# Performance work log

Hardware: AMD Instinct MI355X
Metric: run time of the kernel (lower is better)

Reference implementation:

```python
import jax, jax.numpy as jnp
import numpy as np

N = 100000   # nodes
E = 1600000  # edges
IN, HID, OUT = 128, 128, 64  # hidden = 2 * out_channels per GCNEncoder


def setup_inputs() -> dict:
    key = jax.random.key(0)
    k = jax.random.split(key, 5)
    x = jax.random.normal(k[0], (N, IN), dtype=jnp.float32)
    edge_index = jax.random.randint(k[1], (2, E), 0, N, dtype=jnp.int32)
    # Glorot-style init like PyG GCNConv
    W1 = jax.random.normal(k[2], (IN, HID), dtype=jnp.float32) * (1.0 / np.sqrt(IN))
    b1 = jnp.zeros((HID,), dtype=jnp.float32)
    W2 = jax.random.normal(k[3], (HID, OUT), dtype=jnp.float32) * (1.0 / np.sqrt(HID))
    b2 = jnp.zeros((OUT,), dtype=jnp.float32)
    return {"x": x, "edge_index": edge_index, "W1": W1, "b1": b1, "W2": W2, "b2": b2}


def gcn_conv(x, row, col, W, b):
    # x: [N, F_in]; row/col: [E+N] (edge_index with self-loops appended)
    h = x @ W                                      # dense transform [N, F_out]
    deg = jax.ops.segment_sum(jnp.ones_like(col, dtype=h.dtype), col, num_segments=N)
    dinv = jnp.where(deg > 0, jax.lax.rsqrt(deg), 0.0)
    norm = dinv[row] * dinv[col]                   # symmetric normalization per edge
    msg = h[row] * norm[:, None]                   # gather + scale: [E+N, F_out]
    out = jax.ops.segment_sum(msg, col, num_segments=N)  # scatter-add to targets
    return out + b


def reference(x, edge_index, W1, b1, W2, b2):
    loops = jnp.arange(N, dtype=edge_index.dtype)
    row = jnp.concatenate([edge_index[0], loops])  # sources
    col = jnp.concatenate([edge_index[1], loops])  # targets
    h = jax.nn.relu(gcn_conv(x, row, col, W1, b1))
    return gcn_conv(h, row, col, W2, b2)
```

## Files before the change

### kernel.cpp

```cpp
#include <hip/hip_runtime.h>
#include <hip/hip_fp16.h>

#define N_NODES 100000
#define N_EDGES 1600000
#define K_DIM   128

#define CHUNK_LG 7
#define CHUNK    128
#define NBKT     ((N_NODES + CHUNK - 1) / CHUNK)
#define CAP      2560
#define EPB      4096
#define NBLK_A   ((N_EDGES + EPB - 1) / EPB)
#define G1_BLOCKS ((N_NODES + 63) / 64)
#define NBLK_TOT (G1_BLOCKS + NBLK_A)

typedef _Float16 half8 __attribute__((ext_vector_type(8)));
typedef float    f32x4 __attribute__((ext_vector_type(4)));

__global__ __launch_bounds__(256) void k_prepW(const float* __restrict__ W1,
                                               const float* __restrict__ W2,
                                               _Float16* __restrict__ Wt1,
                                               _Float16* __restrict__ Wt2,
                                               int* __restrict__ gcur) {
    if (blockIdx.x >= 12) {
        int i = (blockIdx.x - 12) * 256 + threadIdx.x;
        if (i < NBKT) gcur[i] = 0;
        return;
    }
    int c = blockIdx.x * 256 + threadIdx.x;
    const float* W; _Float16* Wt; int nout;
    if (c < 2048) { W = W1; Wt = Wt1; nout = 128; }
    else          { W = W2; Wt = Wt2; nout = 64; c -= 2048; }
    int n  = c >> 4;
    int k0 = (c & 15) * 8;
    half8 v;
#pragma unroll
    for (int j = 0; j < 8; ++j)
        v[j] = (_Float16)W[(size_t)(k0 + j) * nout + n];
    *reinterpret_cast<half8*>(Wt + (size_t)n * K_DIM + k0) = v;
}

__global__ __launch_bounds__(256) void k_gemm1_bucket(
    const float* __restrict__ x, const _Float16* __restrict__ Wt,
    _Float16* __restrict__ Hout,
    const int* __restrict__ row, const int* __restrict__ col,
    int* __restrict__ gcur, int* __restrict__ pairs)
{
    __shared__ __align__(16) char smem[128 * 136 * 2];

    if (blockIdx.x % 5 != 0) {
        constexpr int KD = K_DIM, NOUT = 128, NT = NOUT / 16;
        _Float16 (*Blds)[KD + 8] = reinterpret_cast<_Float16(*)[KD + 8]>(smem);

        for (int i = threadIdx.x; i < NOUT * (KD / 8); i += 256) {
            int n = i >> 4, k0 = (i & 15) * 8;
            *reinterpret_cast<half8*>(&Blds[n][k0]) =
                *reinterpret_cast<const half8*>(Wt + (size_t)n * KD + k0);
        }
        __syncthreads();

        const int tile = blockIdx.x - blockIdx.x / 5 - 1;
        const int wave = threadIdx.x >> 6;
        const int lane = threadIdx.x & 63;
        const int r16  = lane & 15;
        const int kg   = lane >> 4;
        const int arow = tile * 64 + wave * 16 + r16;
        const bool rowok = arow < N_NODES;

        f32x4 acc[NT];
#pragma unroll
        for (int ct = 0; ct < NT; ++ct) acc[ct] = (f32x4){0.f, 0.f, 0.f, 0.f};

#pragma unroll
        for (int kc = 0; kc < KD / 32; ++kc) {
            const int k0 = kc * 32 + kg * 8;
            float4 xa = make_float4(0.f, 0.f, 0.f, 0.f), xb = xa;
            if (rowok) {
                const float4* ap = reinterpret_cast<const float4*>(
                    x + (size_t)arow * KD + k0);
                xa = ap[0]; xb = ap[1];
            }
            half8 a;
            a[0] = (_Float16)xa.x; a[1] = (_Float16)xa.y;
            a[2] = (_Float16)xa.z; a[3] = (_Float16)xa.w;
            a[4] = (_Float16)xb.x; a[5] = (_Float16)xb.y;
            a[6] = (_Float16)xb.z; a[7] = (_Float16)xb.w;
#pragma unroll
            for (int ct = 0; ct < NT; ++ct) {
                half8 b = *reinterpret_cast<const half8*>(&Blds[ct * 16 + r16][k0]);
                acc[ct] = __builtin_amdgcn_mfma_f32_16x16x32_f16(a, b, acc[ct], 0, 0, 0);
            }
        }

        const int orow0 = tile * 64 + wave * 16 + kg * 4;
#pragma unroll
        for (int r = 0; r < 4; ++r) {
            int orow = orow0 + r;
            if (orow < N_NODES) {
#pragma unroll
                for (int ct = 0; ct < NT; ++ct)
                    Hout[(size_t)orow * NOUT + ct * 16 + r16] = (_Float16)acc[ct][r];
            }
        }
    } else {
        int* hist  = (int*)smem;
        int* sbase = hist + 1024;
        int* lcur  = hist + 2048;
        int t = threadIdx.x;
        for (int i = t; i < NBKT; i += 256) { hist[i] = 0; lcur[i] = 0; }
        __syncthreads();
        int base = (blockIdx.x / 5) * EPB;
        int myb[16], myp[16];
#pragma unroll
        for (int j = 0; j < 16; ++j) {
            int i = base + t + j * 256;
            int b = -1, p = 0;
            if (i < N_EDGES) {
                int r = row[i], c = col[i];
                b = c >> CHUNK_LG;
                p = ((c & (CHUNK - 1)) << 17) | r;
                atomicAdd(&hist[b], 1);
            }
            myb[j] = b; myp[j] = p;
        }
        __syncthreads();
        for (int i = t; i < NBKT; i += 256) {
            int c = hist[i];
            sbase[i] = c ? atomicAdd(&gcur[i], c) : 0;
        }
        __syncthreads();
#pragma unroll
        for (int j = 0; j < 16; ++j) {
            int b = myb[j];
            if (b >= 0) {
                int pos = sbase[b] + atomicAdd(&lcur[b], 1);
                pairs[(size_t)b * CAP + pos] = myp[j];
            }
        }
    }
}

__global__ __launch_bounds__(256) void k_fillB(const int* __restrict__ gcur,
                                               const int* __restrict__ pairs,
                                               int* __restrict__ rowptr,
                                               float* __restrict__ dinv,
                                               int* __restrict__ srows) {
    __shared__ int mpl[CAP];
    __shared__ int red[256];
    __shared__ int psum[CHUNK];
    __shared__ int deg[CHUNK];
    __shared__ int curs[CHUNK];
    int b = blockIdx.x, t = threadIdx.x;

    int part = 0;
    for (int i = t; i < NBKT; i += 256)
        if (i < b) part += gcur[i];
    red[t] = part;
    if (t < CHUNK) deg[t] = 0;
    __syncthreads();
    for (int off = 128; off; off >>= 1) {
        if (t < off) red[t] += red[t + off];
        __syncthreads();
    }
    int gb = red[0];
    int cnt = gcur[b];
    if (b == 0 && t == 0) rowptr[N_NODES] = N_EDGES;

    const int* mp = pairs + (size_t)b * CAP;

    for (int i = t; i < cnt; i += 256) {
        int v = mp[i];
        mpl[i] = v;
        atomicAdd(&deg[v >> 17], 1);
    }
    __syncthreads();

    int d = (t < CHUNK) ? deg[t] : 0;
    if (t < CHUNK) psum[t] = d;
    __syncthreads();
    for (int off = 1; off < CHUNK; off <<= 1) {
        int u = (t >= off && t < CHUNK) ? psum[t - off] : 0;
        __syncthreads();
        if (t < CHUNK) psum[t] += u;
        __syncthreads();
    }
    if (t < CHUNK) {
        int o = gb + psum[t] - d;
        curs[t] = o;
        int node = (b << CHUNK_LG) + t;
        if (node < N_NODES) {
            rowptr[node] = o;
            dinv[node] = rsqrtf(1.f + (float)d);
        }
    }
    __syncthreads();
    for (int i = t; i < cnt; i += 256) {
        int v = mpl[i];
        int pos = atomicAdd(&curs[v >> 17], 1);
        srows[pos] = v & 0x1FFFF;
    }
}

template<int NOUT>
__global__ __launch_bounds__(256) void k_gemm_mfma2(
    const _Float16* __restrict__ Ah, const _Float16* __restrict__ Wt,
    const float* __restrict__ b_in, _Float16* __restrict__ Hout, int nrows)
{
    constexpr int KD = K_DIM;
    constexpr int NT = NOUT / 16;
    __shared__ _Float16 Blds[NOUT][KD + 8];

    for (int i = threadIdx.x; i < NOUT * (KD / 8); i += 256) {
        int n = i >> 4, k0 = (i & 15) * 8;
        *reinterpret_cast<half8*>(&Blds[n][k0]) =
            *reinterpret_cast<const half8*>(Wt + (size_t)n * KD + k0);
    }
    __syncthreads();

    const int wave = threadIdx.x >> 6;
    const int lane = threadIdx.x & 63;
    const int r16  = lane & 15;
    const int kg   = lane >> 4;
    const int arow = blockIdx.x * 64 + wave * 16 + r16;
    const bool rowok = arow < nrows;

    f32x4 acc[NT];
#pragma unroll
    for (int ct = 0; ct < NT; ++ct) acc[ct] = (f32x4){0.f, 0.f, 0.f, 0.f};

#pragma unroll
    for (int kc = 0; kc < KD / 32; ++kc) {
        const int k0 = kc * 32 + kg * 8;
        uint4 raw = make_uint4(0, 0, 0, 0);
        if (rowok)
            raw = *reinterpret_cast<const uint4*>(Ah + (size_t)arow * KD + k0);
        union { uint4 u; _Float16 h[8]; } U; U.u = raw;
        float4 bA = *reinterpret_cast<const float4*>(b_in + k0);
        float4 bB = *reinterpret_cast<const float4*>(b_in + k0 + 4);
        half8 a;
        a[0] = (_Float16)fmaxf((float)U.h[0] + bA.x, 0.f);
        a[1] = (_Float16)fmaxf((float)U.h[1] + bA.y, 0.f);
        a[2] = (_Float16)fmaxf((float)U.h[2] + bA.z, 0.f);
        a[3] = (_Float16)fmaxf((float)U.h[3] + bA.w, 0.f);
        a[4] = (_Float16)fmaxf((float)U.h[4] + bB.x, 0.f);
        a[5] = (_Float16)fmaxf((float)U.h[5] + bB.y, 0.f);
        a[6] = (_Float16)fmaxf((float)U.h[6] + bB.z, 0.f);
        a[7] = (_Float16)fmaxf((float)U.h[7] + bB.w, 0.f);
#pragma unroll
        for (int ct = 0; ct < NT; ++ct) {
            half8 b = *reinterpret_cast<const half8*>(&Blds[ct * 16 + r16][k0]);
            acc[ct] = __builtin_amdgcn_mfma_f32_16x16x32_f16(a, b, acc[ct], 0, 0, 0);
        }
    }

    const int orow0 = blockIdx.x * 64 + wave * 16 + kg * 4;
#pragma unroll
    for (int r = 0; r < 4; ++r) {
        int orow = orow0 + r;
        if (orow < nrows) {
#pragma unroll
            for (int ct = 0; ct < NT; ++ct)
                Hout[(size_t)orow * NOUT + ct * 16 + r16] = (_Float16)acc[ct][r];
        }
    }
}

__device__ __forceinline__ void fma8(uint4 v, float wgt, float (&acc)[8]) {
    union { uint4 u; _Float16 h[8]; } U;
    U.u = v;
#pragma unroll
    for (int j = 0; j < 8; ++j)
        acc[j] = fmaf((float)U.h[j], wgt, acc[j]);
}

template<int F, bool OUT_HALF>
__global__ __launch_bounds__(256) void k_gather_h(
    const int* __restrict__ rowptr, const int* __restrict__ srows,
    const float* __restrict__ dinv, const _Float16* __restrict__ H,
    const float* __restrict__ bias, void* __restrict__ OUT, int n)
{
    constexpr int LPR = F / 8;
    constexpr int GR  = 32 / LPR;
    int lane = threadIdx.x & 63;
    int half = lane >> 5;
    int hl   = lane & 31;
    int w = blockIdx.x * 8 + (threadIdx.x >> 6) * 2 + half;
    if (w >= n) return;
    int g = hl / LPR;
    int c = hl % LPR;
    float di = dinv[w];
    int s = rowptr[w], e = rowptr[w + 1];
    const uint4* Hp = reinterpret_cast<const uint4*>(H);

    float acc[8];
#pragma unroll
    for (int j = 0; j < 8; ++j) acc[j] = 0.f;
    uint4 hv = Hp[(size_t)w * LPR + c];
    fma8(hv, (g == 0) ? di * di : 0.f, acc);

    if (s < e) {
        int k0 = s + g;
        int kc = min(k0, e - 1);
        int r  = srows[kc];
        float wcur = (k0 < e) ? dinv[r] * di : 0.f;
        uint4 hcur = Hp[(size_t)r * LPR + c];
        for (int k = s + GR; k < e; k += GR) {
            int k1  = k + g;
            int kc1 = min(k1, e - 1);
            int r1  = srows[kc1];
            float wnxt = (k1 < e) ? dinv[r1] * di : 0.f;
            uint4 hnxt = Hp[(size_t)r1 * LPR + c];
            fma8(hcur, wcur, acc);
            wcur = wnxt; hcur = hnxt;
        }
        fma8(hcur, wcur, acc);
    }

#pragma unroll
    for (int m = 16; m >= LPR; m >>= 1) {
#pragma unroll
        for (int j = 0; j < 8; ++j)
            acc[j] += __shfl_xor(acc[j], m, 64);
    }

    if (g == 0) {
        if constexpr (OUT_HALF) {
            union { uint4 u; __half2 h[4]; } P;
#pragma unroll
            for (int j = 0; j < 4; ++j)
                P.h[j] = __floats2half2_rn(acc[2 * j], acc[2 * j + 1]);
            reinterpret_cast<uint4*>(OUT)[(size_t)w * LPR + c] = P.u;
        } else {
            const float4* bp = reinterpret_cast<const float4*>(bias + c * 8);
            float4 b0 = bp[0], b1v = bp[1];
            float4 o0 = make_float4(acc[0] + b0.x, acc[1] + b0.y,
                                    acc[2] + b0.z, acc[3] + b0.w);
            float4 o1 = make_float4(acc[4] + b1v.x, acc[5] + b1v.y,
                                    acc[6] + b1v.z, acc[7] + b1v.w);
            float* op = (float*)OUT + (size_t)w * F + c * 8;
            *reinterpret_cast<float4*>(op)     = o0;
            *reinterpret_cast<float4*>(op + 4) = o1;
        }
    }
}


extern "C" void kernel_launch(void* const* d_in, const int* in_sizes, int n_in,
                              void* d_out, int out_size, void* d_ws, size_t ws_size,
                              hipStream_t stream) {
    const float* x  = (const float*)d_in[0];
    const int*   ei = (const int*)  d_in[1];
    const float* W1 = (const float*)d_in[2];
    const float* b1 = (const float*)d_in[3];
    const float* W2 = (const float*)d_in[4];
    const float* b2 = (const float*)d_in[5];
    float* out = (float*)d_out;

    const int* row = ei;
    const int* col = ei + N_EDGES;

    char* ws = (char*)d_ws;
    int*   gcur   = (int*)ws;
    int*   rowptr = gcur + 1024;
    float* dinv   = (float*)(rowptr + ((N_NODES + 256) & ~255));
    int*   srows  = (int*)(dinv + ((N_NODES + 255) & ~255));
    _Float16* bufH  = (_Float16*)(srows + ((N_EDGES + 255) & ~255));
    _Float16* bufAgg = bufH + (size_t)N_NODES * 128;
    _Float16* bufH2  = bufAgg + (size_t)N_NODES * 128;
    _Float16* Wt1 = bufH2 + (size_t)N_NODES * 64;
    _Float16* Wt2 = Wt1 + 128 * 128;
    int*   pairs  = (int*)(Wt2 + 64 * 128 + 256);

    k_prepW<<<16, 256, 0, stream>>>(W1, W2, Wt1, Wt2, gcur);

    k_gemm1_bucket<<<NBLK_TOT, 256, 0, stream>>>(
        x, Wt1, bufH, row, col, gcur, pairs);

    k_fillB<<<NBKT, 256, 0, stream>>>(gcur, pairs, rowptr, dinv, srows);

    k_gather_h<128, true><<<(N_NODES + 7) / 8, 256, 0, stream>>>(
        rowptr, srows, dinv, bufH, nullptr, bufAgg, N_NODES);

    k_gemm_mfma2<64><<<(N_NODES + 63) / 64, 256, 0, stream>>>(
        bufAgg, Wt2, b1, bufH2, N_NODES);

    k_gather_h<64, false><<<(N_NODES + 7) / 8, 256, 0, stream>>>(
        rowptr, srows, dinv, bufH2, b2, out, N_NODES);
}
```

Baseline: 176.8 us.

## Split GEMM1 tiles across bucket and fill kernels to overlap stages

The first-layer dense transform is now split across two launches. About half of the 64-row tiles run interleaved with the edge-bucketing blocks, and the rest run interleaved with the CSR fill blocks, which were previously a separate kernel. The aim is to give the latency-bound fill stage concurrent compute work so the GPU is not underused, and to balance the block mix in each launch. The cost is that fill blocks now reserve the larger shared-memory allocation, which may reduce occupancy for that path, and both fused kernels carry more branching.

```diff
diff --git a/kernel.cpp b/kernel.cpp
--- a/kernel.cpp
+++ b/kernel.cpp
@@ -12,7 +12,11 @@
 #define EPB      4096
 #define NBLK_A   ((N_EDGES + EPB - 1) / EPB)
 #define G1_BLOCKS ((N_NODES + 63) / 64)
-#define NBLK_TOT (G1_BLOCKS + NBLK_A)
+
+#define K1_TILES 782
+#define K1_TOTAL (3 * NBLK_A)
+#define K2_TILES (G1_BLOCKS - K1_TILES)
+#define K2_TOTAL (NBKT + K2_TILES)
 
 typedef _Float16 half8 __attribute__((ext_vector_type(8)));
 typedef float    f32x4 __attribute__((ext_vector_type(4)));
@@ -40,117 +44,116 @@
     *reinterpret_cast<half8*>(Wt + (size_t)n * K_DIM + k0) = v;
 }
 
-__global__ __launch_bounds__(256) void k_gemm1_bucket(
+
+__device__ __forceinline__ void gemm1_tile(char* smem, int tile,
     const float* __restrict__ x, const _Float16* __restrict__ Wt,
-    _Float16* __restrict__ Hout,
+    _Float16* __restrict__ Hout)
+{
+    constexpr int KD = K_DIM, NOUT = 128, NT = NOUT / 16;
+    _Float16 (*Blds)[KD + 8] = reinterpret_cast<_Float16(*)[KD + 8]>(smem);
+
+    for (int i = threadIdx.x; i < NOUT * (KD / 8); i += 256) {
+        int n = i >> 4, k0 = (i & 15) * 8;
+        *reinterpret_cast<half8*>(&Blds[n][k0]) =
+            *reinterpret_cast<const half8*>(Wt + (size_t)n * KD + k0);
+    }
+    __syncthreads();
+
+    const int wave = threadIdx.x >> 6;
+    const int lane = threadIdx.x & 63;
+    const int r16  = lane & 15;
+    const int kg   = lane >> 4;
+    const int arow = tile * 64 + wave * 16 + r16;
+    const bool rowok = arow < N_NODES;
+
+    f32x4 acc[NT];
+#pragma unroll
+    for (int ct = 0; ct < NT; ++ct) acc[ct] = (f32x4){0.f, 0.f, 0.f, 0.f};
+
+#pragma unroll
+    for (int kc = 0; kc < KD / 32; ++kc) {
+        const int k0 = kc * 32 + kg * 8;
+        float4 xa = make_float4(0.f, 0.f, 0.f, 0.f), xb = xa;
+        if (rowok) {
+            const float4* ap = reinterpret_cast<const float4*>(
+                x + (size_t)arow * KD + k0);
+            xa = ap[0]; xb = ap[1];
+        }
+        half8 a;
+        a[0] = (_Float16)xa.x; a[1] = (_Float16)xa.y;
+        a[2] = (_Float16)xa.z; a[3] = (_Float16)xa.w;
+        a[4] = (_Float16)xb.x; a[5] = (_Float16)xb.y;
+        a[6] = (_Float16)xb.z; a[7] = (_Float16)xb.w;
+#pragma unroll
+        for (int ct = 0; ct < NT; ++ct) {
+            half8 b = *reinterpret_cast<const half8*>(&Blds[ct * 16 + r16][k0]);
+            acc[ct] = __builtin_amdgcn_mfma_f32_16x16x32_f16(a, b, acc[ct], 0, 0, 0);
+        }
+    }
+
+    const int orow0 = tile * 64 + wave * 16 + kg * 4;
+#pragma unroll
+    for (int r = 0; r < 4; ++r) {
+        int orow = orow0 + r;
+        if (orow < N_NODES) {
+#pragma unroll
+            for (int ct = 0; ct < NT; ++ct)
+                Hout[(size_t)orow * NOUT + ct * 16 + r16] = (_Float16)acc[ct][r];
+        }
+    }
+}
+
+__device__ __forceinline__ void bucket_path(char* smem, int bb,
     const int* __restrict__ row, const int* __restrict__ col,
     int* __restrict__ gcur, int* __restrict__ pairs)
 {
-    __shared__ __align__(16) char smem[128 * 136 * 2];
-
-    if (blockIdx.x % 5 != 0) {
-        constexpr int KD = K_DIM, NOUT = 128, NT = NOUT / 16;
-        _Float16 (*Blds)[KD + 8] = reinterpret_cast<_Float16(*)[KD + 8]>(smem);
-
-        for (int i = threadIdx.x; i < NOUT * (KD / 8); i += 256) {
-            int n = i >> 4, k0 = (i & 15) * 8;
-            *reinterpret_cast<half8*>(&Blds[n][k0]) =
-                *reinterpret_cast<const half8*>(Wt + (size_t)n * KD + k0);
-        }
-        __syncthreads();
-
-        const int tile = blockIdx.x - blockIdx.x / 5 - 1;
-        const int wave = threadIdx.x >> 6;
-        const int lane = threadIdx.x & 63;
-        const int r16  = lane & 15;
-        const int kg   = lane >> 4;
-        const int arow = tile * 64 + wave * 16 + r16;
-        const bool rowok = arow < N_NODES;
-
-        f32x4 acc[NT];
-#pragma unroll
-        for (int ct = 0; ct < NT; ++ct) acc[ct] = (f32x4){0.f, 0.f, 0.f, 0.f};
-
-#pragma unroll
-        for (int kc = 0; kc < KD / 32; ++kc) {
-            const int k0 = kc * 32 + kg * 8;
-            float4 xa = make_float4(0.f, 0.f, 0.f, 0.f), xb = xa;
-            if (rowok) {
-                const float4* ap = reinterpret_cast<const float4*>(
-                    x + (size_t)arow * KD + k0);
-                xa = ap[0]; xb = ap[1];
-            }
-            half8 a;
-            a[0] = (_Float16)xa.x; a[1] = (_Float16)xa.y;
-            a[2] = (_Float16)xa.z; a[3] = (_Float16)xa.w;
-            a[4] = (_Float16)xb.x; a[5] = (_Float16)xb.y;
-            a[6] = (_Float16)xb.z; a[7] = (_Float16)xb.w;
-#pragma unroll
-            for (int ct = 0; ct < NT; ++ct) {
-                half8 b = *reinterpret_cast<const half8*>(&Blds[ct * 16 + r16][k0]);
-                acc[ct] = __builtin_amdgcn_mfma_f32_16x16x32_f16(a, b, acc[ct], 0, 0, 0);
-            }
-        }
-
-        const int orow0 = tile * 64 + wave * 16 + kg * 4;
-#pragma unroll
-        for (int r = 0; r < 4; ++r) {
-            int orow = orow0 + r;
-            if (orow < N_NODES) {
-#pragma unroll
-                for (int ct = 0; ct < NT; ++ct)
-                    Hout[(size_t)orow * NOUT + ct * 16 + r16] = (_Float16)acc[ct][r];
-            }
-        }
-    } else {
-        int* hist  = (int*)smem;
-        int* sbase = hist + 1024;
-        int* lcur  = hist + 2048;
-        int t = threadIdx.x;
-        for (int i = t; i < NBKT; i += 256) { hist[i] = 0; lcur[i] = 0; }
-        __syncthreads();
-        int base = (blockIdx.x / 5) * EPB;
-        int myb[16], myp[16];
-#pragma unroll
-        for (int j = 0; j < 16; ++j) {
-            int i = base + t + j * 256;
-            int b = -1, p = 0;
-            if (i < N_EDGES) {
-                int r = row[i], c = col[i];
-                b = c >> CHUNK_LG;
-                p = ((c & (CHUNK - 1)) << 17) | r;
-                atomicAdd(&hist[b], 1);
-            }
-            myb[j] = b; myp[j] = p;
-        }
-        __syncthreads();
-        for (int i = t; i < NBKT; i += 256) {
-            int c = hist[i];
-            sbase[i] = c ? atomicAdd(&gcur[i], c) : 0;
-        }
-        __syncthreads();
-#pragma unroll
-        for (int j = 0; j < 16; ++j) {
-            int b = myb[j];
-            if (b >= 0) {
-                int pos = sbase[b] + atomicAdd(&lcur[b], 1);
-                pairs[(size_t)b * CAP + pos] = myp[j];
-            }
-        }
-    }
-}
-
-__global__ __launch_bounds__(256) void k_fillB(const int* __restrict__ gcur,
-                                               const int* __restrict__ pairs,
-                                               int* __restrict__ rowptr,
-                                               float* __restrict__ dinv,
-                                               int* __restrict__ srows) {
-    __shared__ int mpl[CAP];
-    __shared__ int red[256];
-    __shared__ int psum[CHUNK];
-    __shared__ int deg[CHUNK];
-    __shared__ int curs[CHUNK];
-    int b = blockIdx.x, t = threadIdx.x;
+    int* hist  = (int*)smem;
+    int* sbase = hist + 1024;
+    int* lcur  = hist + 2048;
+    int t = threadIdx.x;
+    for (int i = t; i < NBKT; i += 256) { hist[i] = 0; lcur[i] = 0; }
+    __syncthreads();
+    int base = bb * EPB;
+    int myb[16], myp[16];
+#pragma unroll
+    for (int j = 0; j < 16; ++j) {
+        int i = base + t + j * 256;
+        int b = -1, p = 0;
+        if (i < N_EDGES) {
+            int r = row[i], c = col[i];
+            b = c >> CHUNK_LG;
+            p = ((c & (CHUNK - 1)) << 17) | r;
+            atomicAdd(&hist[b], 1);
+        }
+        myb[j] = b; myp[j] = p;
+    }
+    __syncthreads();
+    for (int i = t; i < NBKT; i += 256) {
+        int c = hist[i];
+        sbase[i] = c ? atomicAdd(&gcur[i], c) : 0;
+    }
+    __syncthreads();
+#pragma unroll
+    for (int j = 0; j < 16; ++j) {
+        int b = myb[j];
+        if (b >= 0) {
+            int pos = sbase[b] + atomicAdd(&lcur[b], 1);
+            pairs[(size_t)b * CAP + pos] = myp[j];
+        }
+    }
+}
+
+__device__ __forceinline__ void fill_path(char* smem, int b,
+    const int* __restrict__ gcur, const int* __restrict__ pairs,
+    int* __restrict__ rowptr, float* __restrict__ dinv,
+    int* __restrict__ srows)
+{
+    int* mpl  = (int*)smem;
+    int* red  = mpl + CAP;
+    int* psum = red + 256;
+    int* deg  = psum + CHUNK;
+    int* curs = deg + CHUNK;
+    int t = threadIdx.x;
 
     int part = 0;
     for (int i = t; i < NBKT; i += 256)
@@ -199,6 +202,35 @@
         int pos = atomicAdd(&curs[v >> 17], 1);
         srows[pos] = v & 0x1FFFF;
     }
+}
+
+__global__ __launch_bounds__(256) void k_stage1(
+    const float* __restrict__ x, const _Float16* __restrict__ Wt,
+    _Float16* __restrict__ Hout,
+    const int* __restrict__ row, const int* __restrict__ col,
+    int* __restrict__ gcur, int* __restrict__ pairs)
+{
+    __shared__ __align__(16) char smem[128 * 136 * 2];
+    int bid = blockIdx.x;
+    if (bid % 3 == 0)
+        bucket_path(smem, bid / 3, row, col, gcur, pairs);
+    else
+        gemm1_tile(smem, (bid / 3) * 2 + (bid % 3) - 1, x, Wt, Hout);
+}
+
+__global__ __launch_bounds__(256) void k_stage2(
+    const float* __restrict__ x, const _Float16* __restrict__ Wt,
+    _Float16* __restrict__ Hout,
+    const int* __restrict__ gcur, const int* __restrict__ pairs,
+    int* __restrict__ rowptr, float* __restrict__ dinv,
+    int* __restrict__ srows)
+{
+    __shared__ __align__(16) char smem[128 * 136 * 2];
+    int bid = blockIdx.x;
+    if ((bid & 1) == 0)
+        fill_path(smem, bid >> 1, gcur, pairs, rowptr, dinv, srows);
+    else
+        gemm1_tile(smem, K1_TILES + (bid >> 1), x, Wt, Hout);
 }
 
 template<int NOUT>
@@ -373,10 +405,11 @@
 
     k_prepW<<<16, 256, 0, stream>>>(W1, W2, Wt1, Wt2, gcur);
 
-    k_gemm1_bucket<<<NBLK_TOT, 256, 0, stream>>>(
+    k_stage1<<<K1_TOTAL, 256, 0, stream>>>(
         x, Wt1, bufH, row, col, gcur, pairs);
 
-    k_fillB<<<NBKT, 256, 0, stream>>>(gcur, pairs, rowptr, dinv, srows);
+    k_stage2<<<K2_TOTAL, 256, 0, stream>>>(
+        x, Wt1, bufH, gcur, pairs, rowptr, dinv, srows);
 
     k_gather_h<128, true><<<(N_NODES + 7) / 8, 256, 0, stream>>>(
         rowptr, srows, dinv, bufH, nullptr, bufAgg, N_NODES);
```

Measured after the change: 183.0 us. 1.03x slower.
